# Kernel tuning notes

Hardware: AMD Instinct MI355X
Metric: run time of the kernel (lower is better)

Reference implementation:

```python
import jax, jax.numpy as jnp
import numpy as np

HIDDEN = 128
HEADS = 4
S = 128          # number of scenes
N = 64           # pedestrians per scene
TOTAL = S * N


def setup_inputs() -> dict:
    key = jax.random.key(0)
    ks = jax.random.split(key, 12)
    h = HIDDEN
    return {
        "node_features": jax.random.normal(ks[0], (TOTAL, h), jnp.float32),
        "positions": jax.random.normal(ks[1], (TOTAL, 2), jnp.float32),
        # rel_pos_encoder: Linear(2, h//2) -> ReLU -> Linear(h//2, h)
        "W1": jax.random.normal(ks[2], (h // 2, 2), jnp.float32) * 0.5,
        "b1": jax.random.normal(ks[3], (h // 2,), jnp.float32) * 0.02,
        "W2": jax.random.normal(ks[4], (h, h // 2), jnp.float32) * (1.0 / np.sqrt(h // 2)),
        "b2": jax.random.normal(ks[5], (h,), jnp.float32) * 0.02,
        # MultiheadAttention packed in-projection (q,k,v stacked) and out-projection
        "in_proj_w": jax.random.normal(ks[6], (3 * h, h), jnp.float32) * (1.0 / np.sqrt(h)),
        "in_proj_b": jax.random.normal(ks[7], (3 * h,), jnp.float32) * 0.02,
        "out_w": jax.random.normal(ks[8], (h, h), jnp.float32) * (1.0 / np.sqrt(h)),
        "out_b": jax.random.normal(ks[9], (h,), jnp.float32) * 0.02,
        # output_proj: Linear(2h, h)
        "proj_w": jax.random.normal(ks[10], (h, 2 * h), jnp.float32) * (1.0 / np.sqrt(2 * h)),
        "proj_b": jax.random.normal(ks[11], (h,), jnp.float32) * 0.02,
        "num_scenes": S,
        "peds_per_scene": N,
    }


def reference(node_features, positions, W1, b1, W2, b2,
              in_proj_w, in_proj_b, out_w, out_b, proj_w, proj_b,
              num_scenes, peds_per_scene):
    h = node_features.shape[-1]
    heads = HEADS
    dh = h // heads
    s, n = num_scenes, peds_per_scene

    feats = node_features.reshape(s, n, h)          # (S, n, h)
    pos = positions.reshape(s, n, 2)                # (S, n, 2)

    # rel[s, i, j] = pos[j] - pos[i]  (matches unsqueeze(0) - unsqueeze(1))
    rel = pos[:, None, :, :] - pos[:, :, None, :]   # (S, n, n, 2)
    rel_enc = jnp.maximum(rel @ W1.T + b1, 0.0) @ W2.T + b2  # (S, n, n, h)

    Wq, Wk, Wv = jnp.split(in_proj_w, 3, axis=0)
    bq, bk, bv = jnp.split(in_proj_b, 3, axis=0)

    # query: each ped i attends over keys j = feats[j] + rel_enc[i, j]
    key_in = feats[:, None, :, :] + rel_enc          # (S, n, n, h)
    q = (feats @ Wq.T + bq).reshape(s, n, heads, dh)             # (S, n, H, dh)
    k = (key_in @ Wk.T + bk).reshape(s, n, n, heads, dh)         # (S, n, n, H, dh)
    v = (key_in @ Wv.T + bv).reshape(s, n, n, heads, dh)

    scores = jnp.einsum('sihd,sijhd->shij', q, k) / np.sqrt(dh)  # (S, H, n, n)
    attn = jax.nn.softmax(scores, axis=-1)
    ctx = jnp.einsum('shij,sijhd->sihd', attn, v).reshape(s, n, h)
    attn_out = ctx @ out_w.T + out_b                              # (S, n, h)

    combined = jnp.concatenate([feats, attn_out], axis=-1)       # (S, n, 2h)
    out = combined @ proj_w.T + proj_b                            # (S, n, h)
    return out.reshape(s * n, h)
```

## Files before the change

### kernel.cpp

```cpp
#include <hip/hip_runtime.h>
#include <hip/hip_bf16.h>


typedef unsigned int u32;
#define SCALE 0.17677669529663689f

__device__ __forceinline__ float bl(u32 u){ union{u32 x; float f;} c; c.x = u << 16; return c.f; }
__device__ __forceinline__ float bh(u32 u){ union{u32 x; float f;} c; c.x = u & 0xffff0000u; return c.f; }
__device__ __forceinline__ u32 pk(float a, float b){
  union{float f; u32 x;} ca, cb; ca.f = a; cb.f = b;
  u32 ua = (ca.x + 0x7fffu + ((ca.x >> 16) & 1u)) >> 16;
  u32 ub = (cb.x + 0x7fffu + ((cb.x >> 16) & 1u)) >> 16;
  return ua | (ub << 16);
}
__device__ __forceinline__ float dot8(uint4 u, float4 f0, float4 f1, float acc){
  acc = fmaf(bl(u.x), f0.x, acc); acc = fmaf(bh(u.x), f0.y, acc);
  acc = fmaf(bl(u.y), f0.z, acc); acc = fmaf(bh(u.y), f0.w, acc);
  acc = fmaf(bl(u.z), f1.x, acc); acc = fmaf(bh(u.z), f1.y, acc);
  acc = fmaf(bl(u.w), f1.z, acc); acc = fmaf(bh(u.w), f1.w, acc);
  return acc;
}
__device__ __forceinline__ void wsync(){
  __builtin_amdgcn_s_waitcnt(0xC07F);
  __builtin_amdgcn_wave_barrier();
}

__global__ __launch_bounds__(256, 2) void ee_setup(
    const float* __restrict__ nf, const float* __restrict__ b2,
    const float* __restrict__ ipw, const float* __restrict__ ipb,
    const float* __restrict__ w2,
    const float* __restrict__ ow, const float* __restrict__ pw,
    float* __restrict__ W2KT, float* __restrict__ W2VT,
    u32* __restrict__ WQB, u32* __restrict__ OWB, u32* __restrict__ PWB,
    u32* __restrict__ KBt, u32* __restrict__ VB)
{
  const int tid = threadIdx.x, b = blockIdx.x;
  const int cg = tid >> 6, l = tid & 63;
  const float2* ipw2 = (const float2*)ipw;
  const float2* ow2  = (const float2*)ow;
  const float2* pw2  = (const float2*)pw;

  if (b >= 544) {
    for (int k = 0; k < 16; ++k) {
      int i = (b - 544) * 4096 + k * 256 + tid;
      if (i < 8192)       { float2 f = ipw2[i];        WQB[i]        = pk(f.x, f.y); }
      else if (i < 16384) { float2 f = ow2[i - 8192];  OWB[i - 8192] = pk(f.x, f.y); }
      else                { float2 f = pw2[i - 16384]; PWB[i - 16384]= pk(f.x, f.y); }
    }
    return;
  }
  if (b >= 512) {
    int t = (b - 512) * 4 + cg;
    int kv = t & 1, e = t >> 1;
    int c0 = 2 * l;
    const float4* rp = (const float4*)ipw + (size_t)(128 + kv * 128 + c0) * 32;
    const float* w2e = w2 + __builtin_amdgcn_readfirstlane(e);
    float a0 = 0.f, a1 = 0.f;
    #pragma unroll 8
    for (int c4 = 0; c4 < 32; ++c4) {
      float4 wa = rp[c4], wb = rp[32 + c4];
      float x0 = w2e[(4 * c4 + 0) * 64];
      float x1 = w2e[(4 * c4 + 1) * 64];
      float x2 = w2e[(4 * c4 + 2) * 64];
      float x3 = w2e[(4 * c4 + 3) * 64];
      a0 = fmaf(wa.x, x0, a0); a0 = fmaf(wa.y, x1, a0);
      a0 = fmaf(wa.z, x2, a0); a0 = fmaf(wa.w, x3, a0);
      a1 = fmaf(wb.x, x0, a1); a1 = fmaf(wb.y, x1, a1);
      a1 = fmaf(wb.z, x2, a1); a1 = fmaf(wb.w, x3, a1);
    }
    float* dst = kv ? W2VT : W2KT;
    ((float2*)dst)[e * 64 + l] = make_float2(a0, a1);
    return;
  }

  const int s = b >> 2, kv = (b >> 1) & 1, hlf = b & 1;
  __shared__ __align__(16) u32 fbS[64][68];
  __shared__ u32 vtS[64][33];
  const float2* nf2 = (const float2*)nf;
  const float2* b22 = (const float2*)b2;

  for (int idx = tid; idx < 4096; idx += 256) {
    int j = idx >> 6, mw = idx & 63;
    float2 f = nf2[((s << 6) + j) * 64 + mw];
    float2 bb = b22[mw];
    fbS[j][mw] = pk(f.x + bb.x, f.y + bb.y);
  }
  __syncthreads();

  uint4 fr[16];
  {
    const uint4* frow = (const uint4*)&fbS[l][0];
    #pragma unroll
    for (int k = 0; k < 16; ++k) fr[k] = frow[k];
  }
  #pragma unroll 1
  for (int p = 0; p < 8; ++p) {
    int c0 = hlf * 64 + cg * 16 + 2 * p;
    int r0 = 128 + kv * 128 + c0;
    const float4* w0 = (const float4*)ipw +
                       (size_t)__builtin_amdgcn_readfirstlane(r0) * 32;
    const float4* w1r = w0 + 32;
    float a0 = ipb[r0], a1 = ipb[r0 + 1];
    #pragma unroll
    for (int k = 0; k < 16; ++k) {
      uint4 F = fr[k];
      float4 wa = w0[2 * k],  wb = w0[2 * k + 1];
      float4 xa = w1r[2 * k], xb = w1r[2 * k + 1];
      float e0 = bl(F.x), e1 = bh(F.x), e2 = bl(F.y), e3 = bh(F.y);
      float e4 = bl(F.z), e5 = bh(F.z), e6 = bl(F.w), e7 = bh(F.w);
      a0 = fmaf(e0, wa.x, a0); a0 = fmaf(e1, wa.y, a0);
      a0 = fmaf(e2, wa.z, a0); a0 = fmaf(e3, wa.w, a0);
      a0 = fmaf(e4, wb.x, a0); a0 = fmaf(e5, wb.y, a0);
      a0 = fmaf(e6, wb.z, a0); a0 = fmaf(e7, wb.w, a0);
      a1 = fmaf(e0, xa.x, a1); a1 = fmaf(e1, xa.y, a1);
      a1 = fmaf(e2, xa.z, a1); a1 = fmaf(e3, xa.w, a1);
      a1 = fmaf(e4, xb.x, a1); a1 = fmaf(e5, xb.y, a1);
      a1 = fmaf(e6, xb.z, a1); a1 = fmaf(e7, xb.w, a1);
    }
    u32 v = pk(a0, a1);
    int cw = hlf * 32 + cg * 8 + p;
    if (kv == 0) KBt[(((s << 6) + cw) << 6) + l] = v;
    else         vtS[l][cg * 8 + p] = v;
  }
  if (kv == 1) {
    __syncthreads();
    int r = tid >> 2, cb = (tid & 3) * 8;
    #pragma unroll
    for (int k = 0; k < 8; ++k)
      VB[(((s << 6) + r) << 6) + hlf * 32 + cb + k] = vtS[r][cb + k];
  }
}

__global__ __launch_bounds__(256, 3) void ee_main(
    const float* __restrict__ nf, const float* __restrict__ pos,
    const float* __restrict__ w1, const float* __restrict__ b1,
    const float* __restrict__ ipb,
    const float* __restrict__ ob, const float* __restrict__ pb,
    const float* __restrict__ W2KT, const float* __restrict__ W2VT,
    const u32* __restrict__ WQB, const u32* __restrict__ OWB,
    const u32* __restrict__ PWB,
    const u32* __restrict__ KBt, const u32* __restrict__ VB,
    float* __restrict__ outp)
{
  __shared__ __align__(16) float pxS[64], pyS[64], w1xS[64], w1yS[64], b1S[64];
  __shared__ __align__(16) float fqS[4][4][132];
  __shared__ __align__(16) float qS [4][4][132];
  __shared__ __align__(16) float qwhS[4][4][4][68];
  __shared__ __align__(16) float atS[4][4][4][68];

  const int tid = threadIdx.x;
  const int s = blockIdx.x >> 2, qt = blockIdx.x & 3;
  const int w = tid >> 6, l = tid & 63;
  const int c0 = 2 * l;

  if (tid < 64) {
    float2 p = ((const float2*)pos)[(s << 6) + tid];
    pxS[tid] = p.x; pyS[tid] = p.y;
    float2 wv = ((const float2*)w1)[tid];
    w1xS[tid] = wv.x; w1yS[tid] = wv.y;
    b1S[tid] = b1[tid];
  }
  __syncthreads();

  int il[4], ig[4];
  #pragma unroll
  for (int t = 0; t < 4; ++t) { il[t] = qt * 16 + 4 * w + t; ig[t] = (s << 6) + il[t]; }

  #pragma unroll
  for (int t = 0; t < 4; ++t)
    *(float2*)&fqS[w][t][c0] = ((const float2*)nf)[ig[t] * 64 + l];
  wsync();

  {
    float2 bq = ((const float2*)ipb)[l];
    float a0[4], a1[4];
    #pragma unroll
    for (int t = 0; t < 4; ++t) { a0[t] = bq.x; a1[t] = bq.y; }
    const uint4* W4 = (const uint4*)WQB;
    #pragma unroll 4
    for (int m8 = 0; m8 < 16; ++m8) {
      uint4 ua = W4[c0 * 16 + m8];
      uint4 ub = W4[(c0 + 1) * 16 + m8];
      #pragma unroll
      for (int t = 0; t < 4; ++t) {
        float4 f0 = *(const float4*)&fqS[w][t][8 * m8];
        float4 f1 = *(const float4*)&fqS[w][t][8 * m8 + 4];
        a0[t] = dot8(ua, f0, f1, a0[t]);
        a1[t] = dot8(ub, f0, f1, a1[t]);
      }
    }
    #pragma unroll
    for (int t = 0; t < 4; ++t)
      *(float2*)&qS[w][t][c0] = make_float2(a0[t], a1[t]);
  }
  wsync();

  {
    const float4* G4 = (const float4*)W2KT;
    #pragma unroll
    for (int hd = 0; hd < 4; ++hd) {
      float acc[4] = {0.f, 0.f, 0.f, 0.f};
      #pragma unroll
      for (int dq = 0; dq < 8; ++dq) {
        float4 g = G4[l * 32 + hd * 8 + dq];
        #pragma unroll
        for (int t = 0; t < 4; ++t) {
          float4 qf = *(const float4*)&qS[w][t][hd * 32 + 4 * dq];
          acc[t] = fmaf(g.x, qf.x, acc[t]); acc[t] = fmaf(g.y, qf.y, acc[t]);
          acc[t] = fmaf(g.z, qf.z, acc[t]); acc[t] = fmaf(g.w, qf.w, acc[t]);
        }
      }
      #pragma unroll
      for (int t = 0; t < 4; ++t) qwhS[w][t][hd][l] = acc[t];
    }
  }
  wsync();

  float at[4][4];
  float pix[4], piy[4];
  {
    float pjx = pxS[l], pjy = pyS[l];
    float rx[4], ry[4];
    #pragma unroll
    for (int t = 0; t < 4; ++t) {
      pix[t] = pxS[il[t]]; piy[t] = pyS[il[t]];
      rx[t] = pjx - pix[t]; ry[t] = pjy - piy[t];
    }
    float sc[4][4];
    #pragma unroll
    for (int t = 0; t < 4; ++t)
      #pragma unroll
      for (int hd = 0; hd < 4; ++hd) sc[t][hd] = 0.f;

    const u32* kbp = KBt + (s << 12);
    #pragma unroll 8
    for (int m2 = 0; m2 < 32; ++m2) {
      u32 u0 = kbp[((2 * m2) << 6) + l];
      u32 u1 = kbp[((2 * m2 + 1) << 6) + l];
      const int hd = m2 >> 3;
      #pragma unroll
      for (int t = 0; t < 4; ++t) {
        float4 qf = *(const float4*)&qS[w][t][4 * m2];
        sc[t][hd] = fmaf(bl(u0), qf.x, sc[t][hd]);
        sc[t][hd] = fmaf(bh(u0), qf.y, sc[t][hd]);
        sc[t][hd] = fmaf(bl(u1), qf.z, sc[t][hd]);
        sc[t][hd] = fmaf(bh(u1), qf.w, sc[t][hd]);
      }
    }
    #pragma unroll 2
    for (int eb = 0; eb < 8; ++eb) {
      float4 wx0 = *(const float4*)&w1xS[8 * eb];
      float4 wx1 = *(const float4*)&w1xS[8 * eb + 4];
      float4 wy0 = *(const float4*)&w1yS[8 * eb];
      float4 wy1 = *(const float4*)&w1yS[8 * eb + 4];
      float4 bb0 = *(const float4*)&b1S[8 * eb];
      float4 bb1 = *(const float4*)&b1S[8 * eb + 4];
      #pragma unroll
      for (int t = 0; t < 4; ++t) {
        float h0 = fmaxf(0.f, fmaf(rx[t], wx0.x, fmaf(ry[t], wy0.x, bb0.x)));
        float h1 = fmaxf(0.f, fmaf(rx[t], wx0.y, fmaf(ry[t], wy0.y, bb0.y)));
        float h2 = fmaxf(0.f, fmaf(rx[t], wx0.z, fmaf(ry[t], wy0.z, bb0.z)));
        float h3 = fmaxf(0.f, fmaf(rx[t], wx0.w, fmaf(ry[t], wy0.w, bb0.w)));
        float h4 = fmaxf(0.f, fmaf(rx[t], wx1.x, fmaf(ry[t], wy1.x, bb1.x)));
        float h5 = fmaxf(0.f, fmaf(rx[t], wx1.y, fmaf(ry[t], wy1.y, bb1.y)));
        float h6 = fmaxf(0.f, fmaf(rx[t], wx1.z, fmaf(ry[t], wy1.z, bb1.z)));
        float h7 = fmaxf(0.f, fmaf(rx[t], wx1.w, fmaf(ry[t], wy1.w, bb1.w)));
        #pragma unroll
        for (int hd = 0; hd < 4; ++hd) {
          float4 q0 = *(const float4*)&qwhS[w][t][hd][8 * eb];
          float4 q1 = *(const float4*)&qwhS[w][t][hd][8 * eb + 4];
          float a = sc[t][hd];
          a = fmaf(q0.x, h0, a); a = fmaf(q0.y, h1, a);
          a = fmaf(q0.z, h2, a); a = fmaf(q0.w, h3, a);
          a = fmaf(q1.x, h4, a); a = fmaf(q1.y, h5, a);
          a = fmaf(q1.z, h6, a); a = fmaf(q1.w, h7, a);
          sc[t][hd] = a;
        }
      }
    }
    #pragma unroll
    for (int t = 0; t < 4; ++t) {
      #pragma unroll
      for (int hd = 0; hd < 4; ++hd) {
        float v = sc[t][hd] * SCALE;
        float m = v;
        #pragma unroll
        for (int off = 32; off > 0; off >>= 1) m = fmaxf(m, __shfl_xor(m, off));
        float p = __expf(v - m);
        float su = p;
        #pragma unroll
        for (int off = 32; off > 0; off >>= 1) su += __shfl_xor(su, off);
#if __has_builtin(__builtin_amdgcn_rcpf)
        at[t][hd] = p * __builtin_amdgcn_rcpf(su);
#else
        at[t][hd] = p / su;
#endif
        atS[w][t][hd][l] = at[t][hd];
      }
    }
  }
  wsync();

  {
    float wx = w1xS[l], wy = w1yS[l], bb = b1S[l];
    float wh[4][4];
    #pragma unroll
    for (int t = 0; t < 4; ++t)
      #pragma unroll
      for (int hd = 0; hd < 4; ++hd) wh[t][hd] = 0.f;
    #pragma unroll 4
    for (int j4 = 0; j4 < 16; ++j4) {
      float4 px = *(const float4*)&pxS[4 * j4];
      float4 py = *(const float4*)&pyS[4 * j4];
      #pragma unroll
      for (int t = 0; t < 4; ++t) {
        float4 a0v = *(const float4*)&atS[w][t][0][4 * j4];
        float4 a1v = *(const float4*)&atS[w][t][1][4 * j4];
        float4 a2v = *(const float4*)&atS[w][t][2][4 * j4];
        float4 a3v = *(const float4*)&atS[w][t][3][4 * j4];
        float h;
        h = fmaxf(0.f, fmaf(px.x - pix[t], wx, fmaf(py.x - piy[t], wy, bb)));
        wh[t][0] = fmaf(a0v.x, h, wh[t][0]); wh[t][1] = fmaf(a1v.x, h, wh[t][1]);
        wh[t][2] = fmaf(a2v.x, h, wh[t][2]); wh[t][3] = fmaf(a3v.x, h, wh[t][3]);
        h = fmaxf(0.f, fmaf(px.y - pix[t], wx, fmaf(py.y - piy[t], wy, bb)));
        wh[t][0] = fmaf(a0v.y, h, wh[t][0]); wh[t][1] = fmaf(a1v.y, h, wh[t][1]);
        wh[t][2] = fmaf(a2v.y, h, wh[t][2]); wh[t][3] = fmaf(a3v.y, h, wh[t][3]);
        h = fmaxf(0.f, fmaf(px.z - pix[t], wx, fmaf(py.z - piy[t], wy, bb)));
        wh[t][0] = fmaf(a0v.z, h, wh[t][0]); wh[t][1] = fmaf(a1v.z, h, wh[t][1]);
        wh[t][2] = fmaf(a2v.z, h, wh[t][2]); wh[t][3] = fmaf(a3v.z, h, wh[t][3]);
        h = fmaxf(0.f, fmaf(px.w - pix[t], wx, fmaf(py.w - piy[t], wy, bb)));
        wh[t][0] = fmaf(a0v.w, h, wh[t][0]); wh[t][1] = fmaf(a1v.w, h, wh[t][1]);
        wh[t][2] = fmaf(a2v.w, h, wh[t][2]); wh[t][3] = fmaf(a3v.w, h, wh[t][3]);
      }
    }
    #pragma unroll
    for (int t = 0; t < 4; ++t)
      #pragma unroll
      for (int hd = 0; hd < 4; ++hd) qwhS[w][t][hd][l] = wh[t][hd];
  }
  wsync();

  {
    const int hd = l >> 4;
    float cx0[4] = {0,0,0,0}, cx1[4] = {0,0,0,0};
    const float2* V2 = (const float2*)W2VT;
    const u32* vbp = VB + (s << 12);
    #pragma unroll 4
    for (int n4 = 0; n4 < 16; ++n4) {
      float2 g0 = V2[((4 * n4 + 0) << 6) + l];
      float2 g1 = V2[((4 * n4 + 1) << 6) + l];
      float2 g2 = V2[((4 * n4 + 2) << 6) + l];
      float2 g3 = V2[((4 * n4 + 3) << 6) + l];
      u32 v0 = vbp[((4 * n4 + 0) << 6) + l];
      u32 v1 = vbp[((4 * n4 + 1) << 6) + l];
      u32 v2 = vbp[((4 * n4 + 2) << 6) + l];
      u32 v3 = vbp[((4 * n4 + 3) << 6) + l];
      #pragma unroll
      for (int t = 0; t < 4; ++t) {
        float4 whv = *(const float4*)&qwhS[w][t][hd][4 * n4];
        float4 atv = *(const float4*)&atS[w][t][hd][4 * n4];
        float a0 = cx0[t], a1 = cx1[t];
        a0 = fmaf(whv.x, g0.x, a0); a1 = fmaf(whv.x, g0.y, a1);
        a0 = fmaf(atv.x, bl(v0), a0); a1 = fmaf(atv.x, bh(v0), a1);
        a0 = fmaf(whv.y, g1.x, a0); a1 = fmaf(whv.y, g1.y, a1);
        a0 = fmaf(atv.y, bl(v1), a0); a1 = fmaf(atv.y, bh(v1), a1);
        a0 = fmaf(whv.z, g2.x, a0); a1 = fmaf(whv.z, g2.y, a1);
        a0 = fmaf(atv.z, bl(v2), a0); a1 = fmaf(atv.z, bh(v2), a1);
        a0 = fmaf(whv.w, g3.x, a0); a1 = fmaf(whv.w, g3.y, a1);
        a0 = fmaf(atv.w, bl(v3), a0); a1 = fmaf(atv.w, bh(v3), a1);
        cx0[t] = a0; cx1[t] = a1;
      }
    }
    wsync();
    #pragma unroll
    for (int t = 0; t < 4; ++t)
      *(float2*)&qS[w][t][c0] = make_float2(cx0[t], cx1[t]);
  }
  wsync();

  {
    float2 b = ((const float2*)ob)[l];
    float a0[4], a1[4];
    #pragma unroll
    for (int t = 0; t < 4; ++t) { a0[t] = b.x; a1[t] = b.y; }
    const uint4* W4 = (const uint4*)OWB;
    #pragma unroll 4
    for (int m8 = 0; m8 < 16; ++m8) {
      uint4 ua = W4[c0 * 16 + m8];
      uint4 ub = W4[(c0 + 1) * 16 + m8];
      #pragma unroll
      for (int t = 0; t < 4; ++t) {
        float4 f0 = *(const float4*)&qS[w][t][8 * m8];
        float4 f1 = *(const float4*)&qS[w][t][8 * m8 + 4];
        a0[t] = dot8(ua, f0, f1, a0[t]);
        a1[t] = dot8(ub, f0, f1, a1[t]);
      }
    }
    wsync();
    #pragma unroll
    for (int t = 0; t < 4; ++t)
      *(float2*)(&qwhS[w][t][0][0] + c0) = make_float2(a0[t], a1[t]);
  }
  wsync();

  {
    float2 b = ((const float2*)pb)[l];
    float a0[4], a1[4];
    #pragma unroll
    for (int t = 0; t < 4; ++t) { a0[t] = b.x; a1[t] = b.y; }
    const uint4* W4 = (const uint4*)PWB;
    #pragma unroll 2
    for (int m8 = 0; m8 < 16; ++m8) {
      uint4 ua = W4[c0 * 32 + m8];
      uint4 ub = W4[(c0 + 1) * 32 + m8];
      uint4 uc = W4[c0 * 32 + 16 + m8];
      uint4 ud = W4[(c0 + 1) * 32 + 16 + m8];
      #pragma unroll
      for (int t = 0; t < 4; ++t) {
        float4 f0 = *(const float4*)&fqS[w][t][8 * m8];
        float4 f1 = *(const float4*)&fqS[w][t][8 * m8 + 4];
        float4 g0 = *(const float4*)(&qwhS[w][t][0][0] + 8 * m8);
        float4 g1 = *(const float4*)(&qwhS[w][t][0][0] + 8 * m8 + 4);
        a0[t] = dot8(ua, f0, f1, a0[t]);
        a1[t] = dot8(ub, f0, f1, a1[t]);
        a0[t] = dot8(uc, g0, g1, a0[t]);
        a1[t] = dot8(ud, g0, g1, a1[t]);
      }
    }
    #pragma unroll
    for (int t = 0; t < 4; ++t)
      ((float2*)outp)[ig[t] * 64 + l] = make_float2(a0[t], a1[t]);
  }
}

extern "C" void kernel_launch(void* const* d_in, const int* in_sizes, int n_in,
                              void* d_out, int out_size, void* d_ws, size_t ws_size,
                              hipStream_t stream) {
  (void)in_sizes; (void)n_in; (void)out_size; (void)ws_size;
  const float* nf  = (const float*)d_in[0];
  const float* pos = (const float*)d_in[1];
  const float* w1  = (const float*)d_in[2];
  const float* b1  = (const float*)d_in[3];
  const float* w2  = (const float*)d_in[4];
  const float* b2  = (const float*)d_in[5];
  const float* ipw = (const float*)d_in[6];
  const float* ipb = (const float*)d_in[7];
  const float* ow  = (const float*)d_in[8];
  const float* ob  = (const float*)d_in[9];
  const float* pw  = (const float*)d_in[10];
  const float* pb  = (const float*)d_in[11];

  char* ws = (char*)d_ws;
  float* W2KT = (float*)(ws);
  float* W2VT = (float*)(ws + (32 << 10));
  u32* WQB  = (u32*)(ws + (64 << 10));
  u32* OWB  = (u32*)(ws + (96 << 10));
  u32* PWB  = (u32*)(ws + (128 << 10));
  u32* KBt  = (u32*)(ws + (192 << 10));
  u32* VB   = (u32*)(ws + (192 << 10) + (128 * 4096 * 4));

  ee_setup<<<dim3(552), dim3(256), 0, stream>>>(nf, b2, ipw, ipb, w2, ow, pw,
                                                W2KT, W2VT, WQB, OWB, PWB, KBt, VB);
  ee_main<<<dim3(512), dim3(256), 0, stream>>>(nf, pos, w1, b1, ipb, ob, pb,
                                               W2KT, W2VT, WQB, OWB, PWB,
                                               KBt, VB, (float*)d_out);
}
```

Baseline: 183.6 us.

## Use packed bf16 dot2 instructions and bf16 activations in shared memory

Activations held in shared memory (query features, q, context, attention output) and the W2K-folded weight are now packed bf16 pairs, and the matvec inner loops use v_dot2_f32_bf16 in place of unpack-plus-fma sequences. This halves LDS traffic for those buffers and cuts the ALU instruction count in the projection, score and output GEMV loops. It adds an extra rounding of intermediates to bf16, which may reduce accuracy. Launch bounds for the main kernel drop from 3 to 2 waves per SIMD.

New measurement: 173.2 us. 5.7% less time.

```diff
diff --git a/kernel.cpp b/kernel.cpp
--- a/kernel.cpp
+++ b/kernel.cpp
@@ -13,11 +13,24 @@
   u32 ub = (cb.x + 0x7fffu + ((cb.x >> 16) & 1u)) >> 16;
   return ua | (ub << 16);
 }
-__device__ __forceinline__ float dot8(uint4 u, float4 f0, float4 f1, float acc){
-  acc = fmaf(bl(u.x), f0.x, acc); acc = fmaf(bh(u.x), f0.y, acc);
-  acc = fmaf(bl(u.y), f0.z, acc); acc = fmaf(bh(u.y), f0.w, acc);
-  acc = fmaf(bl(u.z), f1.x, acc); acc = fmaf(bh(u.z), f1.y, acc);
-  acc = fmaf(bl(u.w), f1.z, acc); acc = fmaf(bh(u.w), f1.w, acc);
+
+#if __has_builtin(__builtin_amdgcn_fdot2_f32_bf16)
+__device__ __forceinline__ float dot2b(u32 a, u32 b, float c){
+  float d;
+  asm("v_dot2_f32_bf16 %0, %1, %2, %3" : "=v"(d) : "v"(a), "v"(b), "v"(c));
+  return d;
+}
+#else
+__device__ __forceinline__ float dot2b(u32 a, u32 b, float c){
+  c = fmaf(bl(a), bl(b), c);
+  return fmaf(bh(a), bh(b), c);
+}
+#endif
+__device__ __forceinline__ float dot8b(uint4 wv, uint4 fv, float acc){
+  acc = dot2b(wv.x, fv.x, acc);
+  acc = dot2b(wv.y, fv.y, acc);
+  acc = dot2b(wv.z, fv.z, acc);
+  acc = dot2b(wv.w, fv.w, acc);
   return acc;
 }
 __device__ __forceinline__ void wsync(){
@@ -30,7 +43,7 @@
     const float* __restrict__ ipw, const float* __restrict__ ipb,
     const float* __restrict__ w2,
     const float* __restrict__ ow, const float* __restrict__ pw,
-    float* __restrict__ W2KT, float* __restrict__ W2VT,
+    u32* __restrict__ W2KB, float* __restrict__ W2VT,
     u32* __restrict__ WQB, u32* __restrict__ OWB, u32* __restrict__ PWB,
     u32* __restrict__ KBt, u32* __restrict__ VB)
 {
@@ -68,8 +81,8 @@
       a1 = fmaf(wb.x, x0, a1); a1 = fmaf(wb.y, x1, a1);
       a1 = fmaf(wb.z, x2, a1); a1 = fmaf(wb.w, x3, a1);
     }
-    float* dst = kv ? W2VT : W2KT;
-    ((float2*)dst)[e * 64 + l] = make_float2(a0, a1);
+    if (kv) ((float2*)W2VT)[e * 64 + l] = make_float2(a0, a1);
+    else    W2KB[e * 64 + l] = pk(a0, a1);
     return;
   }
 
@@ -131,20 +144,20 @@
   }
 }
 
-__global__ __launch_bounds__(256, 3) void ee_main(
+__global__ __launch_bounds__(256, 2) void ee_main(
     const float* __restrict__ nf, const float* __restrict__ pos,
     const float* __restrict__ w1, const float* __restrict__ b1,
     const float* __restrict__ ipb,
     const float* __restrict__ ob, const float* __restrict__ pb,
-    const float* __restrict__ W2KT, const float* __restrict__ W2VT,
+    const u32* __restrict__ W2KB, const float* __restrict__ W2VT,
     const u32* __restrict__ WQB, const u32* __restrict__ OWB,
     const u32* __restrict__ PWB,
     const u32* __restrict__ KBt, const u32* __restrict__ VB,
     float* __restrict__ outp)
 {
   __shared__ __align__(16) float pxS[64], pyS[64], w1xS[64], w1yS[64], b1S[64];
-  __shared__ __align__(16) float fqS[4][4][132];
-  __shared__ __align__(16) float qS [4][4][132];
+  __shared__ __align__(16) u32 fqSu[4][4][68];
+  __shared__ __align__(16) u32 qSu [4][4][68];
   __shared__ __align__(16) float qwhS[4][4][4][68];
   __shared__ __align__(16) float atS[4][4][4][68];
 
@@ -167,8 +180,10 @@
   for (int t = 0; t < 4; ++t) { il[t] = qt * 16 + 4 * w + t; ig[t] = (s << 6) + il[t]; }
 
   #pragma unroll
-  for (int t = 0; t < 4; ++t)
-    *(float2*)&fqS[w][t][c0] = ((const float2*)nf)[ig[t] * 64 + l];
+  for (int t = 0; t < 4; ++t) {
+    float2 f = ((const float2*)nf)[ig[t] * 64 + l];
+    fqSu[w][t][l] = pk(f.x, f.y);
+  }
   wsync();
 
   {
@@ -183,31 +198,29 @@
       uint4 ub = W4[(c0 + 1) * 16 + m8];
       #pragma unroll
       for (int t = 0; t < 4; ++t) {
-        float4 f0 = *(const float4*)&fqS[w][t][8 * m8];
-        float4 f1 = *(const float4*)&fqS[w][t][8 * m8 + 4];
-        a0[t] = dot8(ua, f0, f1, a0[t]);
-        a1[t] = dot8(ub, f0, f1, a1[t]);
-      }
-    }
-    #pragma unroll
-    for (int t = 0; t < 4; ++t)
-      *(float2*)&qS[w][t][c0] = make_float2(a0[t], a1[t]);
-  }
-  wsync();
-
-  {
-    const float4* G4 = (const float4*)W2KT;
+        uint4 fp = *(const uint4*)&fqSu[w][t][4 * m8];
+        a0[t] = dot8b(ua, fp, a0[t]);
+        a1[t] = dot8b(ub, fp, a1[t]);
+      }
+    }
+    #pragma unroll
+    for (int t = 0; t < 4; ++t) qSu[w][t][l] = pk(a0[t], a1[t]);
+  }
+  wsync();
+
+  {
+    const uint2* G2 = (const uint2*)W2KB;
     #pragma unroll
     for (int hd = 0; hd < 4; ++hd) {
       float acc[4] = {0.f, 0.f, 0.f, 0.f};
       #pragma unroll
       for (int dq = 0; dq < 8; ++dq) {
-        float4 g = G4[l * 32 + hd * 8 + dq];
+        uint2 g = G2[l * 32 + hd * 8 + dq];
         #pragma unroll
         for (int t = 0; t < 4; ++t) {
-          float4 qf = *(const float4*)&qS[w][t][hd * 32 + 4 * dq];
-          acc[t] = fmaf(g.x, qf.x, acc[t]); acc[t] = fmaf(g.y, qf.y, acc[t]);
-          acc[t] = fmaf(g.z, qf.z, acc[t]); acc[t] = fmaf(g.w, qf.w, acc[t]);
+          uint2 qp = *(const uint2*)&qSu[w][t][hd * 16 + 2 * dq];
+          acc[t] = dot2b(g.x, qp.x, acc[t]);
+          acc[t] = dot2b(g.y, qp.y, acc[t]);
         }
       }
       #pragma unroll
@@ -240,11 +253,9 @@
       const int hd = m2 >> 3;
       #pragma unroll
       for (int t = 0; t < 4; ++t) {
-        float4 qf = *(const float4*)&qS[w][t][4 * m2];
-        sc[t][hd] = fmaf(bl(u0), qf.x, sc[t][hd]);
-        sc[t][hd] = fmaf(bh(u0), qf.y, sc[t][hd]);
-        sc[t][hd] = fmaf(bl(u1), qf.z, sc[t][hd]);
-        sc[t][hd] = fmaf(bh(u1), qf.w, sc[t][hd]);
+        uint2 qp = *(const uint2*)&qSu[w][t][2 * m2];
+        sc[t][hd] = dot2b(u0, qp.x, sc[t][hd]);
+        sc[t][hd] = dot2b(u1, qp.y, sc[t][hd]);
       }
     }
     #pragma unroll 2
@@ -374,7 +385,7 @@
     wsync();
     #pragma unroll
     for (int t = 0; t < 4; ++t)
-      *(float2*)&qS[w][t][c0] = make_float2(cx0[t], cx1[t]);
+      qSu[w][t][l] = pk(cx0[t], cx1[t]);
   }
   wsync();
 
@@ -390,16 +401,15 @@
       uint4 ub = W4[(c0 + 1) * 16 + m8];
       #pragma unroll
       for (int t = 0; t < 4; ++t) {
-        float4 f0 = *(const float4*)&qS[w][t][8 * m8];
-        float4 f1 = *(const float4*)&qS[w][t][8 * m8 + 4];
-        a0[t] = dot8(ua, f0, f1, a0[t]);
-        a1[t] = dot8(ub, f0, f1, a1[t]);
+        uint4 cp = *(const uint4*)&qSu[w][t][4 * m8];
+        a0[t] = dot8b(ua, cp, a0[t]);
+        a1[t] = dot8b(ub, cp, a1[t]);
       }
     }
     wsync();
     #pragma unroll
     for (int t = 0; t < 4; ++t)
-      *(float2*)(&qwhS[w][t][0][0] + c0) = make_float2(a0[t], a1[t]);
+      ((u32*)&qwhS[w][t][0][0])[l] = pk(a0[t], a1[t]);
   }
   wsync();
 
@@ -417,14 +427,12 @@
       uint4 ud = W4[(c0 + 1) * 32 + 16 + m8];
       #pragma unroll
       for (int t = 0; t < 4; ++t) {
-        float4 f0 = *(const float4*)&fqS[w][t][8 * m8];
-        float4 f1 = *(const float4*)&fqS[w][t][8 * m8 + 4];
-        float4 g0 = *(const float4*)(&qwhS[w][t][0][0] + 8 * m8);
-        float4 g1 = *(const float4*)(&qwhS[w][t][0][0] + 8 * m8 + 4);
-        a0[t] = dot8(ua, f0, f1, a0[t]);
-        a1[t] = dot8(ub, f0, f1, a1[t]);
-        a0[t] = dot8(uc, g0, g1, a0[t]);
-        a1[t] = dot8(ud, g0, g1, a1[t]);
+        uint4 fp = *(const uint4*)&fqSu[w][t][4 * m8];
+        uint4 gp = *(const uint4*)((const u32*)&qwhS[w][t][0][0] + 4 * m8);
+        a0[t] = dot8b(ua, fp, a0[t]);
+        a1[t] = dot8b(ub, fp, a1[t]);
+        a0[t] = dot8b(uc, gp, a0[t]);
+        a1[t] = dot8b(ud, gp, a1[t]);
       }
     }
     #pragma unroll
@@ -451,7 +459,7 @@
   const float* pb  = (const float*)d_in[11];
 
   char* ws = (char*)d_ws;
-  float* W2KT = (float*)(ws);
+  u32*   W2KB = (u32*)(ws);
   float* W2VT = (float*)(ws + (32 << 10));
   u32* WQB  = (u32*)(ws + (64 << 10));
   u32* OWB  = (u32*)(ws + (96 << 10));
@@ -460,8 +468,8 @@
   u32* VB   = (u32*)(ws + (192 << 10) + (128 * 4096 * 4));
 
   ee_setup<<<dim3(552), dim3(256), 0, stream>>>(nf, b2, ipw, ipb, w2, ow, pw,
-                                                W2KT, W2VT, WQB, OWB, PWB, KBt, VB);
+                                                W2KB, W2VT, WQB, OWB, PWB, KBt, VB);
   ee_main<<<dim3(512), dim3(256), 0, stream>>>(nf, pos, w1, b1, ipb, ob, pb,
-                                               W2KT, W2VT, WQB, OWB, PWB,
+                                               W2KB, W2VT, WQB, OWB, PWB,
                                                KBt, VB, (float*)d_out);
 }
```
